# Kernel tuning notes

Hardware: AMD Instinct MI355X
Metric: run time of the kernel (lower is better)

## Reference

```python
import jax, jax.numpy as jnp
import numpy as np

MAX_NORM = 1.0 - 1e-5


def _norm(x):
    return jnp.sqrt(jnp.sum(x * x, axis=-1, keepdims=True) + 1e-15)


def project(x):
    n = _norm(x)
    return jnp.where(n > MAX_NORM, x * (MAX_NORM / n), x)


def artanh(x):
    return jnp.arctanh(jnp.clip(x, -1.0 + 1e-7, 1.0 - 1e-7))


def expmap0(u):
    n = _norm(u)
    return project(jnp.tanh(n) * u / n)


def logmap0(x):
    x = project(x)
    n = _norm(x)
    return artanh(n) * x / n


def mobius_add(x, y):
    x2 = jnp.sum(x * x, -1, keepdims=True)
    y2 = jnp.sum(y * y, -1, keepdims=True)
    xy = jnp.sum(x * y, -1, keepdims=True)
    num = (1.0 + 2.0 * xy + y2) * x + (1.0 - x2) * y
    den = 1.0 + 2.0 * xy + x2 * y2
    return project(num / den)


def mobius_matvec(M, x):
    # M: [d, d]; x: [..., d]  ->  expmap0(M @ logmap0(x))
    return expmap0(jnp.einsum('...d,ed->...e', logmap0(x), M))


def mobius_pw(w, x):
    # pointwise (diagonal) mobius scaling
    return expmap0(w * logmap0(x))


def hyper_gru(seq, Wz, Wr, Wh, Uz, Ur, Uh, bz, br, bh):
    # seq: [S, B, H, d] -> outputs [S, B, H, d]; state is H points per sample in a d-dim Poincare ball
    def cell(h, x):
        z = jax.nn.sigmoid(logmap0(mobius_add(mobius_add(mobius_matvec(Wz, h), mobius_matvec(Uz, x)), bz)))
        r = jax.nn.sigmoid(logmap0(mobius_add(mobius_add(mobius_matvec(Wr, h), mobius_matvec(Ur, x)), br)))
        h_tilde = mobius_add(mobius_add(mobius_matvec(Wh, mobius_pw(r, h)), mobius_matvec(Uh, x)), bh)
        h_new = mobius_add(h, mobius_pw(z, mobius_add(-h, h_tilde)))
        return h_new, h_new
    h0 = jnp.zeros_like(seq[0])
    _, outs = jax.lax.scan(cell, h0, seq)
    return outs


def poinc_dist_sum(enc, lab):
    # enc: [B,S,H,d] (in-ball), lab: [L,H,d] (in-ball) -> sum_H poinc_dist : [B,S,L]
    e2 = jnp.sum(enc * enc, -1)                      # [B,S,H]
    l2 = jnp.sum(lab * lab, -1)                      # [L,H]
    el = jnp.einsum('bshd,lhd->bslh', enc, lab)      # [B,S,L,H] (avoids [B,S,L,H,d] diff)
    d2 = e2[:, :, None, :] + l2[None, None, :, :] - 2.0 * el
    denom = (1.0 - e2)[:, :, None, :] * (1.0 - l2)[None, None, :, :]
    z = 1.0 + 2.0 * d2 / jnp.maximum(denom, 1e-15)
    dist = jnp.arccosh(jnp.maximum(z, 1.0 + 1e-7))
    return jnp.sum(dist, axis=-1)                    # [B,S,L]


def _forward(x, word_embed, label_embed, Wz, Wr, Wh, Uz, Ur, Uh, bz, br, bh, W1, b1, W2, b2):
    we = project(word_embed)[x]                      # [B,S,H,d]
    seq = jnp.transpose(we, (1, 0, 2, 3))            # [S,B,H,d]
    outs = hyper_gru(seq, Wz, Wr, Wh, Uz, Ur, Uh, bz, br, bh)
    enc = jnp.transpose(outs, (0, 1, 2, 3))
    enc = jnp.transpose(outs, (1, 0, 2, 3))          # [B,S,H,d]
    inter = poinc_dist_sum(enc, project(label_embed))  # [B,S,L]
    inter = jnp.transpose(inter, (0, 2, 1))          # [B,L,S]
    h = jax.nn.relu(inter @ W1.T + b1)               # [B,L,S//2]
    out = (h @ W2.T + b2)[..., 0]                    # [B,L]
    return out


def setup_inputs() -> dict:
    key = jax.random.key(0)
    ks = jax.random.split(key, 16)
    B, S, L, H, D, V = 4, 512, 512, 32, 8, 30000
    sc = 1.0 / np.sqrt(D)
    x = jax.random.randint(ks[0], (B, S), 0, V)
    inp = {
        'x': x,
        'word_embed': 0.05 * jax.random.normal(ks[1], (V, H, D), jnp.float32),
        'label_embed': 0.05 * jax.random.normal(ks[2], (L, H, D), jnp.float32),
        'Wz': sc * jax.random.normal(ks[3], (D, D), jnp.float32),
        'Wr': sc * jax.random.normal(ks[4], (D, D), jnp.float32),
        'Wh': sc * jax.random.normal(ks[5], (D, D), jnp.float32),
        'Uz': sc * jax.random.normal(ks[6], (D, D), jnp.float32),
        'Ur': sc * jax.random.normal(ks[7], (D, D), jnp.float32),
        'Uh': sc * jax.random.normal(ks[8], (D, D), jnp.float32),
        'bz': 0.01 * jax.random.normal(ks[9], (D,), jnp.float32),
        'br': 0.01 * jax.random.normal(ks[10], (D,), jnp.float32),
        'bh': 0.01 * jax.random.normal(ks[11], (D,), jnp.float32),
        'W1': jax.random.normal(ks[12], (S // 2, S), jnp.float32) / np.sqrt(S),
        'b1': jnp.zeros((S // 2,), jnp.float32),
        'W2': jax.random.normal(ks[13], (1, S // 2), jnp.float32) / np.sqrt(S // 2),
        'b2': jnp.zeros((1,), jnp.float32),
    }
    return inp


def reference(x, word_embed, label_embed, Wz, Wr, Wh, Uz, Ur, Uh, bz, br, bh, W1, b1, W2, b2):
    return _forward(x, word_embed, label_embed, Wz, Wr, Wh, Uz, Ur, Uh, bz, br, bh, W1, b1, W2, b2)
```

## Files before the change

### kernel.cpp

```cpp
#include <hip/hip_runtime.h>
#include <math.h>

#define DEV __device__ __forceinline__

static constexpr int BB = 4, SS = 512, LL = 512, HH = 32;
static constexpr float MAXN  = 1.0f - 1e-5f;
static constexpr float MAXN2 = MAXN * MAXN;

DEV float rcpf(float x) { return __builtin_amdgcn_rcpf(x); }
DEV float rsqf(float x) { return __builtin_amdgcn_rsqf(x); }

DEV float dot8(const float* a, const float* b) {
  float s0 = a[0]*b[0], s1 = a[1]*b[1], s2 = a[2]*b[2], s3 = a[3]*b[3];
  float s4 = a[4]*b[4], s5 = a[5]*b[5], s6 = a[6]*b[6], s7 = a[7]*b[7];
  return ((s0+s1)+(s2+s3)) + ((s4+s5)+(s6+s7));
}

DEV void load8(float* d, const float* p) {
  float4 a = *(const float4*)p;
  float4 b = *(const float4*)(p + 4);
  d[0]=a.x; d[1]=a.y; d[2]=a.z; d[3]=a.w;
  d[4]=b.x; d[5]=b.y; d[6]=b.z; d[7]=b.w;
}

DEV void store8(float* p, const float* d) {
  *(float4*)p       = make_float4(d[0], d[1], d[2], d[3]);
  *(float4*)(p + 4) = make_float4(d[4], d[5], d[6], d[7]);
}

DEV void project8(float* x) {
  float n2 = dot8(x, x) + 1e-15f;
  if (n2 > MAXN2) {
    float s = MAXN * rsqf(n2);
    #pragma unroll
    for (int i = 0; i < 8; ++i) x[i] *= s;
  }
}

DEV void logmap0_8(float* o, const float* x) {
  float t[8];
  #pragma unroll
  for (int i = 0; i < 8; ++i) t[i] = x[i];
  project8(t);
  float n2 = dot8(t, t) + 1e-15f;
  float rs = rsqf(n2);
  float n  = n2 * rs;
  float c  = fminf(n, 1.0f - 1e-7f);
  float at = 0.34657359f * (__log2f(1.0f + c) - __log2f(1.0f - c));
  float r  = at * rs;
  #pragma unroll
  for (int i = 0; i < 8; ++i) o[i] = t[i] * r;
}

DEV void expmap0_8(float* o, const float* u) {
  float n2 = dot8(u, u) + 1e-15f;
  float rs = rsqf(n2);
  float n  = n2 * rs;
  float e  = __expf(2.0f * n);
  float th = 1.0f - 2.0f * rcpf(e + 1.0f);
  float r  = th * rs;
  #pragma unroll
  for (int i = 0; i < 8; ++i) o[i] = u[i] * r;
  project8(o);
}

DEV void matvec8(float* o, const float* M, const float* u) {
  #pragma unroll
  for (int e = 0; e < 8; ++e) o[e] = dot8(M + 8*e, u);
}

template<int CTRL>
DEV float dppf(float x) {
  int xi = __float_as_int(x);
  return __int_as_float(__builtin_amdgcn_update_dpp(xi, xi, CTRL, 0xF, 0xF, true));
}

DEV float grp8sum(float x) {
  x += dppf<0xB1>(x);
  x += dppf<0x4E>(x);
  x += dppf<0x141>(x);
  return x;
}

DEV void red2(float& a, float& b) {
  float t0 = dppf<0xB1>(a),  t1 = dppf<0xB1>(b);  a += t0; b += t1;
  float t2 = dppf<0x4E>(a),  t3 = dppf<0x4E>(b);  a += t2; b += t3;
  float t4 = dppf<0x141>(a), t5 = dppf<0x141>(b); a += t4; b += t5;
}

DEV void red4(float& a, float& b, float& c, float& d) {
  float t0 = dppf<0xB1>(a),  t1 = dppf<0xB1>(b),  t2 = dppf<0xB1>(c),  t3 = dppf<0xB1>(d);
  a += t0; b += t1; c += t2; d += t3;
  float t4 = dppf<0x4E>(a),  t5 = dppf<0x4E>(b),  t6 = dppf<0x4E>(c),  t7 = dppf<0x4E>(d);
  a += t4; b += t5; c += t6; d += t7;
  float t8 = dppf<0x141>(a), t9 = dppf<0x141>(b), ta = dppf<0x141>(c), tb = dppf<0x141>(d);
  a += t8; b += t9; c += ta; d += tb;
}

DEV void red5(float& a, float& b, float& c, float& d, float& e) {
  float t0 = dppf<0xB1>(a),  t1 = dppf<0xB1>(b),  t2 = dppf<0xB1>(c),  t3 = dppf<0xB1>(d),  t4 = dppf<0xB1>(e);
  a += t0; b += t1; c += t2; d += t3; e += t4;
  float u0 = dppf<0x4E>(a),  u1 = dppf<0x4E>(b),  u2 = dppf<0x4E>(c),  u3 = dppf<0x4E>(d),  u4 = dppf<0x4E>(e);
  a += u0; b += u1; c += u2; d += u3; e += u4;
  float v0 = dppf<0x141>(a), v1 = dppf<0x141>(b), v2 = dppf<0x141>(c), v3 = dppf<0x141>(d), v4 = dppf<0x141>(e);
  a += v0; b += v1; c += v2; d += v3; e += v4;
}

#define MV8(w, u0,u1,u2,u3,u4,u5,u6,u7) \
  ((((w[0]*(u0)) + (w[1]*(u1))) + ((w[2]*(u2)) + (w[3]*(u3)))) + \
   (((w[4]*(u4)) + (w[5]*(u5))) + ((w[6]*(u6)) + (w[7]*(u7)))))

DEV float lgscale(float n2) {
  float n2p = n2 + 1e-15f;
  float rs  = rsqf(n2p);
  float n   = n2p * rs;
  float at  = 0.34657359f * (__log2f(1.0f + n) - __log2f(1.0f - n));
  return at * rs;
}

DEV void gate1(float n2v, float dvc, float dvb,
               float c2, float b2, float b2p1, float cb,
               float& P, float& Q, float& R, float& g2_2) {
  float n2p = n2v + 1e-15f;
  float rsv = rsqf(n2p);
  float nv  = n2p * rsv;
  float ew  = __expf(2.0f * nv);
  float th  = 1.0f - 2.0f * rcpf(ew + 1.0f);
  float asc = th * rsv;
  float a2  = fminf(th * th, MAXN2);
  float xy1 = asc * dvc;
  float ab  = asc * dvb;
  float x2  = 2.0f * xy1;
  float cx1 = 1.0f + x2 + c2;
  float cy1 = 1.0f - a2;
  float D1  = 1.0f + x2 + a2 * c2;
  float N1  = (cx1*a2)*cx1 + (2.0f*cx1)*(cy1*xy1) + (cy1*c2)*cy1;
  float G   = cx1*ab + cy1*cb;
  float C2  = D1*b2p1 + 2.0f*G;
  float D1q = D1*D1;
  float D2  = D1q + 2.0f*(G*D1) + N1*b2;
  float K   = D1q - N1;
  float E   = rcpf(D2);
  float CE  = C2 * E;
  P = (CE * cx1) * asc;
  Q = CE * cy1;
  R = K * E;
  float g2n = (C2*N1)*C2 + 2.0f*(C2*K)*G + (K*b2)*K;
  g2_2 = fminf(g2n * (E*E), MAXN2);
}

__global__ void prep_kernel(const int* __restrict__ x, const float* __restrict__ wemb,
                            const float* __restrict__ Uz, const float* __restrict__ Ur,
                            const float* __restrict__ Uh,
                            const float* __restrict__ bzp, const float* __restrict__ brp,
                            const float* __restrict__ bhp,
                            float* __restrict__ pkV, float* __restrict__ pkS)
{
  int t = blockIdx.x * 256 + threadIdx.x;
  if (t >= BB * SS * HH) return;
  int hh = t & (HH - 1);
  int bs = t >> 5;
  int idx = x[bs];
  float we[8]; load8(we, wemb + ((size_t)idx * HH + hh) * 8);
  project8(we);
  float lx[8]; logmap0_8(lx, we);
  float bz[8], br[8], bh[8];
  load8(bz, bzp); load8(br, brp); load8(bh, bhp);
  float v[8], az[8], ar[8], ah[8];
  matvec8(v, Uz, lx); expmap0_8(az, v);
  matvec8(v, Ur, lx); expmap0_8(ar, v);
  matvec8(v, Uh, lx); expmap0_8(ah, v);
  float cz2 = dot8(az, az), cr2 = dot8(ar, ar), ch2 = dot8(ah, ah);
  float czb = dot8(az, bz), crb = dot8(ar, br), chb = dot8(ah, bh);
  float2* pv = (float2*)(pkV + (size_t)t * 32);
  #pragma unroll
  for (int j = 0; j < 8; ++j) {
    pv[j]     = make_float2(az[j], ah[j]);
    pv[8 + j] = make_float2(ar[j], ah[j]);
  }
  float4* ps = (float4*)(pkS + (size_t)t * 8);
  ps[0] = make_float4(cz2, czb, ch2, chb);
  ps[1] = make_float4(cr2, crb, ch2, chb);
}

__global__ void label_kernel(const float* __restrict__ lemb,
                             float* __restrict__ labP, float* __restrict__ l2o)
{
  int t = blockIdx.x * 256 + threadIdx.x;
  if (t >= LL * HH) return;
  float lv[8]; load8(lv, lemb + (size_t)t * 8);
  project8(lv);
  store8(labP + (size_t)t * 8, lv);
  l2o[t] = dot8(lv, lv);
}

__global__ __launch_bounds__(64, 1) void gru_kernel(
    const float* __restrict__ Wzp, const float* __restrict__ Wrp, const float* __restrict__ Whp,
    const float* __restrict__ bzp, const float* __restrict__ brp, const float* __restrict__ bhp,
    const float* __restrict__ pkV, const float* __restrict__ pkS,
    float* __restrict__ enc, float* __restrict__ e2out)
{
  const int lane = threadIdx.x;
  const int d    = lane & 7;
  const bool hif = (lane & 8) != 0;
  const int cg   = lane >> 4;
  const int l16  = lane & 15;

  float wg[8], wh[8];
  #pragma unroll
  for (int k = 0; k < 8; ++k) {
    wg[k] = (hif ? Wrp : Wzp)[d*8 + (d^k)];
    wh[k] = Whp[d*8 + (d^k)];
  }
  float bgv = (hif ? brp : bzp)[d];
  float bhv = bhp[d];
  float bg2 = grp8sum(bgv*bgv);
  float bh2 = grp8sum(bhv*bhv);
  float bg2p1 = 1.0f + bg2, bh2p1 = 1.0f + bh2;

  const int chain = blockIdx.x * 4 + cg;
  int soff = (chain >> 5) * SS * HH + (chain & 31);
  int pvo  = soff * 32 + l16 * 2;
  int pso  = soff * 8 + (hif ? 4 : 0);
  int voff = soff * 8 + d;

  float hv = 0.0f, h2 = 0.0f;
  float2 cv = *(const float2*)(pkV + pvo);
  float4 ss = *(const float4*)(pkS + pso);

  #pragma unroll 1
  for (int s = 0; s < SS; ++s) {
    float2 ncv = *(const float2*)(pkV + (pvo + HH*32));
    float4 nss = *(const float4*)(pkS + (pso + HH*8));

    float cgv = cv.x, chv = cv.y;
    float c2g = ss.x, cbg = ss.y, ch2v = ss.z, chbv = ss.w;

    float p1 = dppf<0xB1>(hv), p2 = dppf<0x4E>(hv), p3 = dppf<0x1B>(hv), p7 = dppf<0x141>(hv);
    float p4 = dppf<0x1B>(p7), p5 = dppf<0x4E>(p7), p6 = dppf<0xB1>(p7);
    float vg0 = MV8(wg, hv, p1, p2, p3, p4, p5, p6, p7);

    float w0 = wh[0]*hv, w1 = wh[1]*p1, w2 = wh[2]*p2, w3 = wh[3]*p3;
    float w4 = wh[4]*p4, w5 = wh[5]*p5, w6 = wh[6]*p6, w7 = wh[7]*p7;

    float n2g0 = vg0*vg0, dgc0 = vg0*cgv, dgb0 = vg0*bgv;
    float dhch = hv*chv, dhbh = hv*bhv;
    red5(n2g0, dgc0, dgb0, dhch, dhbh);

    float lsc = lgscale(h2);
    float l2s = lsc * lsc;

    float P, Q, R, g22;
    gate1(n2g0*l2s, dgc0*lsc, dgb0*lsc, c2g, bg2, bg2p1, cbg, P, Q, R, g22);
    float g2 = (P*lsc)*vg0 + Q*cgv + R*bgv;

    float g22p = g22 + 1e-15f;
    float rsg  = rsqf(g22p);
    float ng   = g22p * rsg;
    float Lm   = __log2f(1.0f - ng), Lp = __log2f(1.0f + ng);
    float sarg = (0.34657359f * g2) * rsg * (Lm - Lp);
    float gsv  = rcpf(1.0f + __expf(sarg));
    float gsw  = dppf<0x128>(gsv);
    float rv   = hif ? gsv : gsw;
    float zv   = hif ? gsw : gsv;

    float r1 = dppf<0xB1>(rv), r2 = dppf<0x4E>(rv), r3 = dppf<0x1B>(rv), r7 = dppf<0x141>(rv);
    float r4 = dppf<0x1B>(r7), r5 = dppf<0x4E>(r7), r6 = dppf<0xB1>(r7);
    float vh0 = (((w0*rv + w1*r1) + (w2*r2 + w3*r3)) + ((w4*r4 + w5*r5) + (w6*r6 + w7*r7)));

    float n2h0 = vh0*vh0, rhc0 = vh0*chv, rhb0 = vh0*bhv, dhv0 = hv*vh0;
    red4(n2h0, rhc0, rhb0, dhv0);

    float Ph, Qh, Rh, t42;
    gate1(n2h0*l2s, rhc0*lsc, rhb0*lsc, ch2v, bh2, bh2p1, chbv, Ph, Qh, Rh, t42);
    float Phl  = Ph * lsc;
    float t4   = Phl*vh0 + Qh*chv + Rh*bhv;
    float dht4 = Phl*dhv0 + Qh*dhch + Rh*dhbh;

    float cxm  = 1.0f - 2.0f*dht4 + t42;
    float cym  = 1.0f - h2;
    float denm = 1.0f - 2.0f*dht4 + h2*t42;
    float rdm  = rcpf(denm);
    float m20  = (cxm*h2)*cxm - (2.0f*cxm)*(cym*dht4) + (cym*t42)*cym;
    float m2   = fminf(m20 * (rdm*rdm), MAXN2);
    float lmm  = lgscale(m2);
    float LR   = lmm * rdm;

    float md0 = cym*t4 - cxm*hv;
    float wv0 = zv * md0;
    float n2w0 = wv0*wv0, dhw0 = hv*wv0;
    red2(n2w0, dhw0);
    float n2wp = n2w0 + 1e-15f;
    float rs0  = rsqf(n2wp);
    float nw0  = n2wp * rs0;

    float ewt = __expf((2.0f*LR) * nw0);
    float th2 = 1.0f - 2.0f * rcpf(ewt + 1.0f);
    float W2  = th2 * rs0;
    float ee2 = fminf((W2*W2)*n2w0, MAXN2);

    float xyf  = W2 * dhw0;
    float cxf  = 1.0f + 2.0f*xyf + ee2;
    float denf = 1.0f + 2.0f*xyf + h2*ee2;
    float rdf  = rcpf(denf);
    float A    = rdf * cxf;
    float C    = (rdf * cym) * W2;
    float hn   = A*hv + C*wv0;
    float hn2  = fminf(((cxf*h2)*cxf + (2.0f*cxf)*(cym*xyf) + (cym*ee2)*cym) * (rdf*rdf), MAXN2);

    enc[voff]   = hn;
    e2out[soff] = hn2;

    hv = hn; h2 = hn2;
    cv = ncv; ss = nss;
    pvo += HH*32; pso += HH*8; voff += HH*8; soff += HH;
  }
}

DEV float pdist(float ee, float ll, float el) {
  float d2  = ee + ll - 2.0f * el;
  float den = fmaxf((1.0f - ee) * (1.0f - ll), 1e-15f);
  float z   = 1.0f + 2.0f * d2 * rcpf(den);
  z = fmaxf(z, 1.0f + 1e-7f);
  return 0.69314718f * __log2f(z + sqrtf(z*z - 1.0f));
}

__global__ __launch_bounds__(256) void dist_kernel(
    const float* __restrict__ enc, const float* __restrict__ e2,
    const float* __restrict__ labP, const float* __restrict__ l2,
    float* __restrict__ inter)
{
  int blk = blockIdx.x;
  int lt = blk & 15, st = (blk >> 4) & 15, b = blk >> 8;
  int li = threadIdx.x & 15, si = threadIdx.x >> 4;
  int s = st * 32 + si * 2, l = lt * 32 + li * 2;

  const float* er0 = enc + ((size_t)b * SS + s) * HH * 8;
  const float* er1 = er0 + HH * 8;
  const float* e20 = e2 + ((size_t)b * SS + s) * HH;
  const float* e21 = e20 + HH;
  const float* lr0 = labP + (size_t)l * HH * 8;
  const float* lr1 = lr0 + HH * 8;
  const float* l20 = l2 + (size_t)l * HH;
  const float* l21 = l20 + HH;

  float a00 = 0.f, a01 = 0.f, a10 = 0.f, a11 = 0.f;
  #pragma unroll 2
  for (int hh = 0; hh < HH; ++hh) {
    float ev0[8], ev1[8], lv0[8], lv1[8];
    load8(ev0, er0 + hh * 8); load8(ev1, er1 + hh * 8);
    load8(lv0, lr0 + hh * 8); load8(lv1, lr1 + hh * 8);
    float x00 = dot8(ev0, lv0), x01 = dot8(ev0, lv1);
    float x10 = dot8(ev1, lv0), x11 = dot8(ev1, lv1);
    float e0v = e20[hh], e1v = e21[hh], l0v = l20[hh], l1v = l21[hh];
    a00 += pdist(e0v, l0v, x00);
    a01 += pdist(e0v, l1v, x01);
    a10 += pdist(e1v, l0v, x10);
    a11 += pdist(e1v, l1v, x11);
  }
  float* o0 = inter + ((size_t)b * LL + l) * SS + s;
  o0[0] = a00; o0[1] = a10;
  o0[SS] = a01; o0[SS + 1] = a11;
}

__global__ __launch_bounds__(256) void mlp1_kernel(
    const float* __restrict__ inter, const float* __restrict__ W1,
    const float* __restrict__ b1, float* __restrict__ hbuf)
{
  __shared__ float As[32][33];
  __shared__ float Bs[32][33];
  int t = threadIdx.x;
  int nt = blockIdx.x & 7, mt = blockIdx.x >> 3;
  int row0 = mt * 32, j0 = nt * 32;
  int li = t >> 4, ji = t & 15;
  float acc00 = 0.f, acc01 = 0.f, acc10 = 0.f, acc11 = 0.f;

  for (int k0 = 0; k0 < 512; k0 += 32) {
    __syncthreads();
    {
      int l = t >> 3, kk = (t & 7) * 4;
      float4 v = *(const float4*)(inter + (size_t)(row0 + l) * 512 + k0 + kk);
      As[l][kk] = v.x; As[l][kk+1] = v.y; As[l][kk+2] = v.z; As[l][kk+3] = v.w;
      float4 w = *(const float4*)(W1 + (size_t)(j0 + l) * 512 + k0 + kk);
      Bs[kk][l] = w.x; Bs[kk+1][l] = w.y; Bs[kk+2][l] = w.z; Bs[kk+3][l] = w.w;
    }
    __syncthreads();
    #pragma unroll
    for (int kk = 0; kk < 32; ++kk) {
      float a0 = As[li][kk],  a1 = As[li + 16][kk];
      float b0 = Bs[kk][ji],  b1v = Bs[kk][ji + 16];
      acc00 = fmaf(a0, b0, acc00);
      acc01 = fmaf(a0, b1v, acc01);
      acc10 = fmaf(a1, b0, acc10);
      acc11 = fmaf(a1, b1v, acc11);
    }
  }
  float bj0 = b1[j0 + ji], bj1 = b1[j0 + ji + 16];
  hbuf[(size_t)(row0 + li)      * 256 + j0 + ji]      = fmaxf(acc00 + bj0, 0.f);
  hbuf[(size_t)(row0 + li)      * 256 + j0 + ji + 16] = fmaxf(acc01 + bj1, 0.f);
  hbuf[(size_t)(row0 + li + 16) * 256 + j0 + ji]      = fmaxf(acc10 + bj0, 0.f);
  hbuf[(size_t)(row0 + li + 16) * 256 + j0 + ji + 16] = fmaxf(acc11 + bj1, 0.f);
}

__global__ void mlp2_kernel(const float* __restrict__ hbuf, const float* __restrict__ W2,
                            const float* __restrict__ b2, float* __restrict__ out)
{
  int t = threadIdx.x;
  int row = blockIdx.x * 4 + (t >> 6);
  int lane = t & 63;
  float v = 0.f;
  #pragma unroll
  for (int p = 0; p < 4; ++p) {
    int j = lane + p * 64;
    v = fmaf(hbuf[(size_t)row * 256 + j], W2[j], v);
  }
  #pragma unroll
  for (int off = 32; off > 0; off >>= 1) v += __shfl_xor(v, off);
  if (lane == 0) out[row] = v + b2[0];
}

extern "C" void kernel_launch(void* const* d_in, const int* in_sizes, int n_in,
                              void* d_out, int out_size, void* d_ws, size_t ws_size,
                              hipStream_t stream) {
  (void)in_sizes; (void)n_in; (void)out_size; (void)ws_size;
  const int*   x    = (const int*)d_in[0];
  const float* wemb = (const float*)d_in[1];
  const float* lemb = (const float*)d_in[2];
  const float* Wz = (const float*)d_in[3];
  const float* Wr = (const float*)d_in[4];
  const float* Wh = (const float*)d_in[5];
  const float* Uz = (const float*)d_in[6];
  const float* Ur = (const float*)d_in[7];
  const float* Uh = (const float*)d_in[8];
  const float* bz = (const float*)d_in[9];
  const float* br = (const float*)d_in[10];
  const float* bh = (const float*)d_in[11];
  const float* W1 = (const float*)d_in[12];
  const float* b1 = (const float*)d_in[13];
  const float* W2 = (const float*)d_in[14];
  const float* b2 = (const float*)d_in[15];
  float* out = (float*)d_out;

  float* p = (float*)d_ws;
  const size_t NBSH  = (size_t)BB * SS * HH;
  float* pkV  = p; p += NBSH * 32;
  float* pkS  = p; p += NBSH * 8;
  float* enc  = p; p += NBSH * 8;
  float* e2   = p; p += NBSH;
  float* labP = p; p += (size_t)LL * HH * 8;
  float* l2   = p; p += (size_t)LL * HH;
  float* inter= p; p += (size_t)BB * LL * SS;
  float* hbuf = p; p += (size_t)BB * LL * 256;

  prep_kernel <<<(BB * SS * HH) / 256, 256, 0, stream>>>(x, wemb, Uz, Ur, Uh, bz, br, bh,
                                                         pkV, pkS);
  label_kernel<<<(LL * HH) / 256, 256, 0, stream>>>(lemb, labP, l2);
  gru_kernel  <<<32, 64, 0, stream>>>(Wz, Wr, Wh, bz, br, bh, pkV, pkS, enc, e2);
  dist_kernel <<<BB * (SS / 32) * (LL / 32), 256, 0, stream>>>(enc, e2, labP, l2, inter);
  mlp1_kernel <<<512, 256, 0, stream>>>(inter, W1, b1, hbuf);
  mlp2_kernel <<<512, 256, 0, stream>>>(hbuf, W2, b2, out);
}
```

Baseline: 520.7 us.

## Pack two GRU chains per 16-lane group to halve GRU grid

Each 16-lane group now advances two recurrence chains instead of one. The z and r gate computations are split so that each half-group computes both gates for its own chain, with DPP swaps exchanging the results. The GRU kernel launches 16 blocks instead of 32. The aim is to use the lanes that previously duplicated gate work, but each lane now does more sequential work per step, which lengthens the latency-bound critical path of the recurrence.

```diff
diff --git a/kernel.cpp b/kernel.cpp
--- a/kernel.cpp
+++ b/kernel.cpp
@@ -218,61 +218,93 @@
   float bh2 = grp8sum(bhv*bhv);
   float bg2p1 = 1.0f + bg2, bh2p1 = 1.0f + bh2;
 
-  const int chain = blockIdx.x * 4 + cg;
-  int soff = (chain >> 5) * SS * HH + (chain & 31);
-  int pvo  = soff * 32 + l16 * 2;
-  int pso  = soff * 8 + (hif ? 4 : 0);
-  int voff = soff * 8 + d;
+  const int cLo = blockIdx.x * 8 + cg;
+  const int cHi = cLo + 4;
+  int sfLo = (cLo >> 5) * SS * HH + (cLo & 31);
+  int sfHi = (cHi >> 5) * SS * HH + (cHi & 31);
+  int pvLo = sfLo * 32 + l16 * 2, pvHi = sfHi * 32 + l16 * 2;
+  int psLo = sfLo * 8 + (hif ? 4 : 0), psHi = sfHi * 8 + (hif ? 4 : 0);
+  int sfSelf = hif ? sfHi : sfLo;
+  int voff = sfSelf * 8 + d;
+  int soff = sfSelf;
 
   float hv = 0.0f, h2 = 0.0f;
-  float2 cv = *(const float2*)(pkV + pvo);
-  float4 ss = *(const float4*)(pkS + pso);
+  float2 LA = *(const float2*)(pkV + pvLo);
+  float2 LB = *(const float2*)(pkV + pvHi);
+  float4 SA = *(const float4*)(pkS + psLo);
+  float4 SB = *(const float4*)(pkS + psHi);
 
   #pragma unroll 1
   for (int s = 0; s < SS; ++s) {
-    float2 ncv = *(const float2*)(pkV + (pvo + HH*32));
-    float4 nss = *(const float4*)(pkS + (pso + HH*8));
-
-    float cgv = cv.x, chv = cv.y;
-    float c2g = ss.x, cbg = ss.y, ch2v = ss.z, chbv = ss.w;
-
-    float p1 = dppf<0xB1>(hv), p2 = dppf<0x4E>(hv), p3 = dppf<0x1B>(hv), p7 = dppf<0x141>(hv);
-    float p4 = dppf<0x1B>(p7), p5 = dppf<0x4E>(p7), p6 = dppf<0xB1>(p7);
-    float vg0 = MV8(wg, hv, p1, p2, p3, p4, p5, p6, p7);
-
-    float w0 = wh[0]*hv, w1 = wh[1]*p1, w2 = wh[2]*p2, w3 = wh[3]*p3;
-    float w4 = wh[4]*p4, w5 = wh[5]*p5, w6 = wh[6]*p6, w7 = wh[7]*p7;
-
-    float n2g0 = vg0*vg0, dgc0 = vg0*cgv, dgb0 = vg0*bgv;
-    float dhch = hv*chv, dhbh = hv*bhv;
-    red5(n2g0, dgc0, dgb0, dhch, dhbh);
-
-    float lsc = lgscale(h2);
-    float l2s = lsc * lsc;
-
-    float P, Q, R, g22;
-    gate1(n2g0*l2s, dgc0*lsc, dgb0*lsc, c2g, bg2, bg2p1, cbg, P, Q, R, g22);
-    float g2 = (P*lsc)*vg0 + Q*cgv + R*bgv;
-
-    float g22p = g22 + 1e-15f;
-    float rsg  = rsqf(g22p);
-    float ng   = g22p * rsg;
-    float Lm   = __log2f(1.0f - ng), Lp = __log2f(1.0f + ng);
-    float sarg = (0.34657359f * g2) * rsg * (Lm - Lp);
-    float gsv  = rcpf(1.0f + __expf(sarg));
-    float gsw  = dppf<0x128>(gsv);
-    float rv   = hif ? gsv : gsw;
-    float zv   = hif ? gsw : gsv;
-
-    float r1 = dppf<0xB1>(rv), r2 = dppf<0x4E>(rv), r3 = dppf<0x1B>(rv), r7 = dppf<0x141>(rv);
-    float r4 = dppf<0x1B>(r7), r5 = dppf<0x4E>(r7), r6 = dppf<0xB1>(r7);
-    float vh0 = (((w0*rv + w1*r1) + (w2*r2 + w3*r3)) + ((w4*r4 + w5*r5) + (w6*r6 + w7*r7)));
+    float2 nLA = *(const float2*)(pkV + (pvLo + HH*32));
+    float2 nLB = *(const float2*)(pkV + (pvHi + HH*32));
+    float4 nSA = *(const float4*)(pkS + (psLo + HH*8));
+    float4 nSB = *(const float4*)(pkS + (psHi + HH*8));
+
+    float lsc   = lgscale(h2);
+    float lscSw = dppf<0x128>(lsc);
+    float lsc1  = hif ? lscSw : lsc;
+    float lsc2  = hif ? lsc : lscSw;
+
+    float hvSw = dppf<0x128>(hv);
+    float hv1  = hif ? hvSw : hv;
+    float hv2  = hif ? hv : hvSw;
+
+    float p1 = dppf<0xB1>(hv1), p2 = dppf<0x4E>(hv1), p3 = dppf<0x1B>(hv1), p7 = dppf<0x141>(hv1);
+    float p4 = dppf<0x1B>(p7),  p5 = dppf<0x4E>(p7),  p6 = dppf<0xB1>(p7);
+    float vgA = MV8(wg, hv1, p1, p2, p3, p4, p5, p6, p7);
+    float n2gA = vgA*vgA, dgcA = vgA*LA.x, dgbA = vgA*bgv;
+    float dhcA = hv1*LA.y, dhbA = hv1*bhv;
+    red5(n2gA, dgcA, dgbA, dhcA, dhbA);
+
+    float q1 = dppf<0xB1>(hv2), q2 = dppf<0x4E>(hv2), q3 = dppf<0x1B>(hv2), q7 = dppf<0x141>(hv2);
+    float q4 = dppf<0x1B>(q7),  q5 = dppf<0x4E>(q7),  q6 = dppf<0xB1>(q7);
+    float vgB = MV8(wg, hv2, q1, q2, q3, q4, q5, q6, q7);
+    float n2gB = vgB*vgB, dgcB = vgB*LB.x, dgbB = vgB*bgv;
+    float dhcB = hv2*LB.y, dhbB = hv2*bhv;
+    red5(n2gB, dgcB, dgbB, dhcB, dhbB);
+
+    float P1,Q1,R1,g22A;
+    gate1(n2gA*(lsc1*lsc1), dgcA*lsc1, dgbA*lsc1, SA.x, bg2, bg2p1, SA.y, P1,Q1,R1,g22A);
+    float g2A   = (P1*lsc1)*vgA + Q1*LA.x + R1*bgv;
+    float g22Ap = g22A + 1e-15f;
+    float rsgA  = rsqf(g22Ap);
+    float ngA   = g22Ap * rsgA;
+    float sargA = (0.34657359f * g2A) * rsgA * (__log2f(1.0f - ngA) - __log2f(1.0f + ngA));
+    float gsv1  = rcpf(1.0f + __expf(sargA));
+
+    float P2,Q2,R2,g22B;
+    gate1(n2gB*(lsc2*lsc2), dgcB*lsc2, dgbB*lsc2, SB.x, bg2, bg2p1, SB.y, P2,Q2,R2,g22B);
+    float g2B   = (P2*lsc2)*vgB + Q2*LB.x + R2*bgv;
+    float g22Bp = g22B + 1e-15f;
+    float rsgB  = rsqf(g22Bp);
+    float ngB   = g22Bp * rsgB;
+    float sargB = (0.34657359f * g2B) * rsgB * (__log2f(1.0f - ngB) - __log2f(1.0f + ngB));
+    float gsv2  = rcpf(1.0f + __expf(sargB));
+
+    float sw1 = dppf<0x128>(gsv1), sw2 = dppf<0x128>(gsv2);
+    float zv = hif ? sw2 : gsv1;
+    float rv = hif ? gsv2 : sw1;
+
+    float chv  = hif ? LB.y : LA.y;
+    float ch2v = hif ? SB.z : SA.z;
+    float chbv = hif ? SB.w : SA.w;
+    float dhch = hif ? dhcB : dhcA;
+    float dhbh = hif ? dhbB : dhbA;
+
+    float w0 = wh[0]*hv;
+    float w1 = wh[1]*(hif?q1:p1), w2 = wh[2]*(hif?q2:p2), w3 = wh[3]*(hif?q3:p3);
+    float w4 = wh[4]*(hif?q4:p4), w5 = wh[5]*(hif?q5:p5), w6 = wh[6]*(hif?q6:p6), w7 = wh[7]*(hif?q7:p7);
+
+    float r1_ = dppf<0xB1>(rv), r2_ = dppf<0x4E>(rv), r3_ = dppf<0x1B>(rv), r7_ = dppf<0x141>(rv);
+    float r4_ = dppf<0x1B>(r7_), r5_ = dppf<0x4E>(r7_), r6_ = dppf<0xB1>(r7_);
+    float vh0 = (((w0*rv + w1*r1_) + (w2*r2_ + w3*r3_)) + ((w4*r4_ + w5*r5_) + (w6*r6_ + w7*r7_)));
 
     float n2h0 = vh0*vh0, rhc0 = vh0*chv, rhb0 = vh0*bhv, dhv0 = hv*vh0;
     red4(n2h0, rhc0, rhb0, dhv0);
 
-    float Ph, Qh, Rh, t42;
-    gate1(n2h0*l2s, rhc0*lsc, rhb0*lsc, ch2v, bh2, bh2p1, chbv, Ph, Qh, Rh, t42);
+    float Ph,Qh,Rh,t42;
+    gate1(n2h0*(lsc*lsc), rhc0*lsc, rhb0*lsc, ch2v, bh2, bh2p1, chbv, Ph,Qh,Rh,t42);
     float Phl  = Ph * lsc;
     float t4   = Phl*vh0 + Qh*chv + Rh*bhv;
     float dht4 = Phl*dhv0 + Qh*dhch + Rh*dhbh;
@@ -286,8 +318,8 @@
     float lmm  = lgscale(m2);
     float LR   = lmm * rdm;
 
-    float md0 = cym*t4 - cxm*hv;
-    float wv0 = zv * md0;
+    float md0  = cym*t4 - cxm*hv;
+    float wv0  = zv * md0;
     float n2w0 = wv0*wv0, dhw0 = hv*wv0;
     red2(n2w0, dhw0);
     float n2wp = n2w0 + 1e-15f;
@@ -312,8 +344,9 @@
     e2out[soff] = hn2;
 
     hv = hn; h2 = hn2;
-    cv = ncv; ss = nss;
-    pvo += HH*32; pso += HH*8; voff += HH*8; soff += HH;
+    LA = nLA; LB = nLB; SA = nSA; SB = nSB;
+    pvLo += HH*32; pvHi += HH*32; psLo += HH*8; psHi += HH*8;
+    voff += HH*8; soff += HH;
   }
 }
 
@@ -455,7 +488,7 @@
   prep_kernel <<<(BB * SS * HH) / 256, 256, 0, stream>>>(x, wemb, Uz, Ur, Uh, bz, br, bh,
                                                          pkV, pkS);
   label_kernel<<<(LL * HH) / 256, 256, 0, stream>>>(lemb, labP, l2);
-  gru_kernel  <<<32, 64, 0, stream>>>(Wz, Wr, Wh, bz, br, bh, pkV, pkS, enc, e2);
+  gru_kernel  <<<16, 64, 0, stream>>>(Wz, Wr, Wh, bz, br, bh, pkV, pkS, enc, e2);
   dist_kernel <<<BB * (SS / 32) * (LL / 32), 256, 0, stream>>>(enc, e2, labP, l2, inter);
   mlp1_kernel <<<512, 256, 0, stream>>>(inter, W1, b1, hbuf);
   mlp2_kernel <<<512, 256, 0, stream>>>(hbuf, W2, b2, out);
```

Result: slower. 667.6 us (+28.2%).
